# Optimization experiments

Measured on AMD Instinct MI355X. Metric: run time of the kernel, lower is better.

Reference implementation:

```python
import jax, jax.numpy as jnp
import numpy as np

N_HEADS = 8
OUT_DIM = 256   # node_dim + time_dim
KEY_DIM = 384   # node_dim + edge_dim + time_dim
HEAD_DIM = OUT_DIM // N_HEADS
LN_EPS = 1e-5


def setup_inputs() -> dict:
    key = jax.random.key(0)
    ks = jax.random.split(key, 12)
    B, N, D = 8192, 32, 128
    s = lambda fan_in: 1.0 / np.sqrt(fan_in)
    return {
        "node_feat": jax.random.normal(ks[0], (B, D), jnp.float32),
        "time_feat": jax.random.normal(ks[1], (B, D), jnp.float32),
        "edge_feat": jax.random.normal(ks[2], (B, N, D), jnp.float32),
        "nbr_node_feat": jax.random.normal(ks[3], (B, N, D), jnp.float32),
        "nbr_time_feat": jax.random.normal(ks[4], (B, N, D), jnp.float32),
        "nbr_mask": jax.random.randint(ks[5], (B, N), 0, 2, jnp.int64),
        # parameters, stored as [in, out] so y = x @ W
        "W_Q": jax.random.uniform(ks[6], (OUT_DIM, OUT_DIM), jnp.float32, -s(OUT_DIM), s(OUT_DIM)),
        "W_KV": jax.random.uniform(ks[7], (KEY_DIM, 2 * OUT_DIM), jnp.float32, -s(KEY_DIM), s(KEY_DIM)),
        "W_O": jax.random.uniform(ks[8], (OUT_DIM, OUT_DIM), jnp.float32, -s(OUT_DIM), s(OUT_DIM)),
        "b_O": jax.random.uniform(ks[9], (OUT_DIM,), jnp.float32, -s(OUT_DIM), s(OUT_DIM)),
        "ln_gamma": jnp.ones((OUT_DIM,), jnp.float32),
        "ln_beta": jnp.zeros((OUT_DIM,), jnp.float32),
    }


def reference(node_feat, time_feat, edge_feat, nbr_node_feat, nbr_time_feat,
              nbr_mask, W_Q, W_KV, W_O, b_O, ln_gamma, ln_beta):
    B = node_feat.shape[0]
    # query/residual: [B, out_dim] (query length is 1)
    R = jnp.concatenate([node_feat, time_feat], axis=1)
    Q = (R @ W_Q).reshape(B, N_HEADS, HEAD_DIM)                    # [B,H,d]
    Z = jnp.concatenate([nbr_node_feat, edge_feat, nbr_time_feat], axis=-1) @ W_KV  # [B,N,2*out]
    K = Z[:, :, :OUT_DIM].reshape(B, -1, N_HEADS, HEAD_DIM)        # [B,N,H,d]
    V = Z[:, :, OUT_DIM:].reshape(B, -1, N_HEADS, HEAD_DIM)
    A = jnp.einsum("bhd,bnhd->bhn", Q, K) * (HEAD_DIM ** -0.5)    # [B,H,N]
    masked = (nbr_mask == 0)[:, None, :]                           # [B,1,N]
    A = jnp.where(masked, jnp.float32(-1e10), A)
    A = jax.nn.softmax(A, axis=-1)                                 # dropout is identity (eval / p used at inference off)
    O = jnp.einsum("bhn,bnhd->bhd", A, V).reshape(B, OUT_DIM)
    out = O @ W_O + b_O
    x = out + R
    mu = jnp.mean(x, axis=-1, keepdims=True)
    var = jnp.mean(jnp.square(x - mu), axis=-1, keepdims=True)
    return (x - mu) * jax.lax.rsqrt(var + LN_EPS) * ln_gamma + ln_beta
```

## Files before the change

kernel.cpp:

```cpp
#include <hip/hip_runtime.h>

typedef __attribute__((ext_vector_type(8))) short bf16x8;
typedef __attribute__((ext_vector_type(4))) float f32x4;

#define MSTRIDE 264
#define XSTRIDE 392

__device__ __align__(16) unsigned short g_WQT[256 * 256];
__device__ __align__(16) unsigned short g_WKVT[512 * 384];
__device__ __align__(16) unsigned short g_WOT[256 * 256];

__device__ __forceinline__ float b2f(unsigned short u) {
    union { unsigned int i; float f; } v; v.i = ((unsigned int)u) << 16; return v.f;
}
__device__ __forceinline__ unsigned short f2b(float f) {
    union { float f; unsigned int i; } v; v.f = f;
    unsigned int x = v.i;
    return (unsigned short)((x + 0x7fffu + ((x >> 16) & 1u)) >> 16);
}

__global__ void transcvt_all(const float* __restrict__ wq, const float* __restrict__ wkv,
                             const float* __restrict__ wo,
                             unsigned short* __restrict__ dq, unsigned short* __restrict__ dkv,
                             unsigned short* __restrict__ dwo) {
    __shared__ float tile[32][33];
    const int b = blockIdx.x;
    const float* src; unsigned short* dst; int R, C, bx, by;
    if (b < 64)       { src = wq;  dst = dq;  R = 256; C = 256; bx = b & 7;  by = b >> 3; }
    else if (b < 256) { const int t = b - 64;  src = wkv; dst = dkv; R = 384; C = 512; bx = t & 15; by = t >> 4; }
    else              { const int t = b - 256; src = wo;  dst = dwo; R = 256; C = 256; bx = t & 7;  by = t >> 3; }
    const int c0 = bx * 32, r0 = by * 32;
    const int tx = threadIdx.x, ty = threadIdx.y;
#pragma unroll
    for (int i = 0; i < 32; i += 8)
        tile[ty + i][tx] = src[(size_t)(r0 + ty + i) * C + (c0 + tx)];
    __syncthreads();
#pragma unroll
    for (int i = 0; i < 32; i += 8)
        dst[(size_t)(c0 + ty + i) * R + (r0 + tx)] = f2b(tile[tx][ty + i]);
}

__device__ __forceinline__ void ld8f(const float* __restrict__ s, unsigned short* dst) {
    const float4 a = *(const float4*)s;
    const float4 b = *(const float4*)(s + 4);
    unsigned short t[8];
    t[0] = f2b(a.x); t[1] = f2b(a.y); t[2] = f2b(a.z); t[3] = f2b(a.w);
    t[4] = f2b(b.x); t[5] = f2b(b.y); t[6] = f2b(b.z); t[7] = f2b(b.w);
    *(uint4*)dst = *(const uint4*)t;
}

__global__ __launch_bounds__(256, 2) void ta_fused(
    const float* __restrict__ node,
    const float* __restrict__ timef,
    const float* __restrict__ edge,
    const float* __restrict__ nbrnode,
    const float* __restrict__ nbrtime,
    const int* __restrict__ nmask,
    const float* __restrict__ bO,
    const float* __restrict__ gam,
    const float* __restrict__ bet,
    float* __restrict__ out)
{
    __shared__ __align__(16) unsigned short Xs[64 * XSTRIDE];
    __shared__ __align__(16) unsigned short Rb[16 * MSTRIDE];
    __shared__ __align__(16) unsigned short Ob[16 * MSTRIDE];
    __shared__ float Qs[2][256];
    __shared__ float lnb[2][256];
    __shared__ int   mk[2][32];

    const int gb0  = blockIdx.x * 2;
    const int tid  = threadIdx.x;
    const int w    = tid >> 6;
    const int lane = tid & 63;
    const int l15  = lane & 15;
    const int quad = lane >> 4;

    int orv = 0;
#pragma unroll
    for (int i = 1; i < 64; i += 2) orv |= nmask[i];
    const bool m64 = (orv == 0);

    {
        unsigned int* pO = (unsigned int*)Ob;
        for (int i = tid; i < 16 * MSTRIDE / 2; i += 256) pO[i] = 0u;
        unsigned int* pR = (unsigned int*)Rb;
        for (int i = tid + MSTRIDE; i < 16 * MSTRIDE / 2; i += 256) pR[i] = 0u;
    }
    if (tid < 64) {
        const int b = tid >> 5, s = tid & 31;
        if (s < 16) ld8f(node  + (size_t)(gb0 + b) * 128 + s * 8,        &Rb[b * MSTRIDE + s * 8]);
        else        ld8f(timef + (size_t)(gb0 + b) * 128 + (s - 16) * 8, &Rb[b * MSTRIDE + s * 8]);
    } else if (tid < 128) {
        const int t = tid - 64, b = t >> 5, n = t & 31;
        const size_t j = (size_t)(gb0 + b) * 32 + n;
        mk[b][n] = m64 ? nmask[2 * j] : nmask[j];
    }
#pragma unroll
    for (int i = 0; i < 12; i++) {
        const int g  = i * 256 + tid;
        const int r  = g / 48, c8 = g % 48;
        const float* base; int koff;
        if (c8 < 16)      { base = nbrnode; koff = c8 * 8; }
        else if (c8 < 32) { base = edge;    koff = (c8 - 16) * 8; }
        else              { base = nbrtime; koff = (c8 - 32) * 8; }
        ld8f(base + (size_t)(gb0 * 32 + r) * 128 + koff, &Xs[r * XSTRIDE + c8 * 8]);
    }

    const unsigned short* wq  = g_WQT  + (size_t)(w * 64 + l15) * 256 + quad * 8;
    const unsigned short* wkv = g_WKVT + (size_t)(w * 64 + l15) * 384 + quad * 8;
    const unsigned short* wo  = g_WOT  + (size_t)(w * 64 + l15) * 256 + quad * 8;
    bf16x8 bq[2][4], bK[2][4], bV[2][4];
#pragma unroll
    for (int p = 0; p < 2; p++)
#pragma unroll
        for (int ct = 0; ct < 4; ct++)
            bq[p][ct] = *(const bf16x8*)(wq + (size_t)(ct * 16) * 256 + p * 32);
#pragma unroll
    for (int ct = 0; ct < 4; ct++) {
        bK[0][ct] = *(const bf16x8*)(wkv + (size_t)(ct * 16) * 384);
        bV[0][ct] = *(const bf16x8*)(wkv + (size_t)(256 + ct * 16) * 384);
    }

    __syncthreads();

    const f32x4 zero4 = {0.0f, 0.0f, 0.0f, 0.0f};

    f32x4 accq[4];
#pragma unroll
    for (int ct = 0; ct < 4; ct++) accq[ct] = zero4;
    {
        bf16x8 aq[2];
        aq[0] = *(const bf16x8*)(&Rb[l15 * MSTRIDE + 0 * 32 + quad * 8]);
        aq[1] = *(const bf16x8*)(&Rb[l15 * MSTRIDE + 1 * 32 + quad * 8]);
#pragma unroll
        for (int kc = 0; kc < 8; kc++) {
            const int s = kc & 1;
#pragma unroll
            for (int ct = 0; ct < 4; ct++)
                accq[ct] = __builtin_amdgcn_mfma_f32_16x16x32_bf16(aq[s], bq[s][ct], accq[ct], 0, 0, 0);
            if (kc + 2 < 8) {
                aq[s] = *(const bf16x8*)(&Rb[l15 * MSTRIDE + (kc + 2) * 32 + quad * 8]);
#pragma unroll
                for (int ct = 0; ct < 4; ct++)
                    bq[s][ct] = *(const bf16x8*)(wq + (size_t)(ct * 16) * 256 + (kc + 2) * 32);
            }
        }
    }
    if (quad == 0) {
#pragma unroll
        for (int ct = 0; ct < 4; ct++) {
            Qs[0][w * 64 + ct * 16 + l15] = accq[ct][0];
            Qs[1][w * 64 + ct * 16 + l15] = accq[ct][1];
        }
    }

    f32x4 accK[4][4], accV[4][4];
#pragma unroll
    for (int rt = 0; rt < 4; rt++)
#pragma unroll
        for (int ct = 0; ct < 4; ct++) { accK[rt][ct] = zero4; accV[rt][ct] = zero4; }
    {
        bf16x8 af[2][4];
#pragma unroll
        for (int rt = 0; rt < 4; rt++)
            af[0][rt] = *(const bf16x8*)(&Xs[(rt * 16 + l15) * XSTRIDE + quad * 8]);
#pragma unroll
        for (int ct = 0; ct < 4; ct++) {
            bK[1][ct] = *(const bf16x8*)(wkv + (size_t)(ct * 16) * 384 + 32);
            bV[1][ct] = *(const bf16x8*)(wkv + (size_t)(256 + ct * 16) * 384 + 32);
        }
#pragma unroll
        for (int kc = 0; kc < 12; kc++) {
            const int s = kc & 1;
            if (kc + 1 < 12) {
#pragma unroll
                for (int rt = 0; rt < 4; rt++)
                    af[s ^ 1][rt] = *(const bf16x8*)(&Xs[(rt * 16 + l15) * XSTRIDE + (kc + 1) * 32 + quad * 8]);
            }
            __builtin_amdgcn_s_setprio(1);
#pragma unroll
            for (int ct = 0; ct < 4; ct++)
#pragma unroll
                for (int rt = 0; rt < 4; rt++) {
                    accK[rt][ct] = __builtin_amdgcn_mfma_f32_16x16x32_bf16(af[s][rt], bK[s][ct], accK[rt][ct], 0, 0, 0);
                    accV[rt][ct] = __builtin_amdgcn_mfma_f32_16x16x32_bf16(af[s][rt], bV[s][ct], accV[rt][ct], 0, 0, 0);
                }
            __builtin_amdgcn_s_setprio(0);
            if (kc + 2 < 12) {
#pragma unroll
                for (int ct = 0; ct < 4; ct++) {
                    bK[s][ct] = *(const bf16x8*)(wkv + (size_t)(ct * 16) * 384 + (kc + 2) * 32);
                    bV[s][ct] = *(const bf16x8*)(wkv + (size_t)(256 + ct * 16) * 384 + (kc + 2) * 32);
                }
            }
        }
    }

    bf16x8 bo[2][4];
#pragma unroll
    for (int p = 0; p < 2; p++)
#pragma unroll
        for (int ct = 0; ct < 4; ct++)
            bo[p][ct] = *(const bf16x8*)(wo + (size_t)(ct * 16) * 256 + p * 32);

    float aw[2][2][2][4];
    const float scl = 0.17677669529663687f;
#pragma unroll
    for (int bb = 0; bb < 2; bb++) {
        float qv[4];
#pragma unroll
        for (int ct = 0; ct < 4; ct++) qv[ct] = Qs[bb][w * 64 + ct * 16 + l15];
#pragma unroll
        for (int hl = 0; hl < 2; hl++) {
            float sv[2][4];
#pragma unroll
            for (int rtl = 0; rtl < 2; rtl++) {
                const int rt = bb * 2 + rtl;
#pragma unroll
                for (int rg = 0; rg < 4; rg++)
                    sv[rtl][rg] = accK[rt][2 * hl][rg] * qv[2 * hl]
                                + accK[rt][2 * hl + 1][rg] * qv[2 * hl + 1];
            }
#pragma unroll
            for (int m = 1; m <= 8; m <<= 1)
#pragma unroll
                for (int rtl = 0; rtl < 2; rtl++)
#pragma unroll
                    for (int rg = 0; rg < 4; rg++)
                        sv[rtl][rg] += __shfl_xor(sv[rtl][rg], m, 64);
            float mx = -3.0e38f;
#pragma unroll
            for (int rtl = 0; rtl < 2; rtl++)
#pragma unroll
                for (int rg = 0; rg < 4; rg++) {
                    const int n = rtl * 16 + quad * 4 + rg;
                    sv[rtl][rg] = (mk[bb][n] != 0) ? sv[rtl][rg] * scl : -1.0e10f;
                    mx = fmaxf(mx, sv[rtl][rg]);
                }
            mx = fmaxf(mx, __shfl_xor(mx, 16, 64));
            mx = fmaxf(mx, __shfl_xor(mx, 32, 64));
            float sum = 0.0f;
#pragma unroll
            for (int rtl = 0; rtl < 2; rtl++)
#pragma unroll
                for (int rg = 0; rg < 4; rg++) {
                    const float e = __expf(sv[rtl][rg] - mx);
                    aw[bb][hl][rtl][rg] = e;
                    sum += e;
                }
            sum += __shfl_xor(sum, 16, 64);
            sum += __shfl_xor(sum, 32, 64);
            const float inv = 1.0f / sum;
#pragma unroll
            for (int rtl = 0; rtl < 2; rtl++)
#pragma unroll
                for (int rg = 0; rg < 4; rg++)
                    aw[bb][hl][rtl][rg] *= inv;
        }
    }

#pragma unroll
    for (int bb = 0; bb < 2; bb++)
#pragma unroll
        for (int hl = 0; hl < 2; hl++)
#pragma unroll
            for (int ctl = 0; ctl < 2; ctl++) {
                const int ct = hl * 2 + ctl;
                float o = 0.0f;
#pragma unroll
                for (int rtl = 0; rtl < 2; rtl++)
#pragma unroll
                    for (int rg = 0; rg < 4; rg++)
                        o += aw[bb][hl][rtl][rg] * accV[bb * 2 + rtl][ct][rg];
                o += __shfl_xor(o, 16, 64);
                o += __shfl_xor(o, 32, 64);
                if (quad == 0) {
                    const int col = (w * 2 + hl) * 32 + ctl * 16 + l15;
                    Ob[bb * MSTRIDE + col] = f2b(o);
                }
            }
    __syncthreads();

    f32x4 acco[4];
#pragma unroll
    for (int ct = 0; ct < 4; ct++) acco[ct] = zero4;
    {
        bf16x8 ao[2];
        ao[0] = *(const bf16x8*)(&Ob[l15 * MSTRIDE + 0 * 32 + quad * 8]);
        ao[1] = *(const bf16x8*)(&Ob[l15 * MSTRIDE + 1 * 32 + quad * 8]);
#pragma unroll
        for (int kc = 0; kc < 8; kc++) {
            const int s = kc & 1;
#pragma unroll
            for (int ct = 0; ct < 4; ct++)
                acco[ct] = __builtin_amdgcn_mfma_f32_16x16x32_bf16(ao[s], bo[s][ct], acco[ct], 0, 0, 0);
            if (kc + 2 < 8) {
                ao[s] = *(const bf16x8*)(&Ob[l15 * MSTRIDE + (kc + 2) * 32 + quad * 8]);
#pragma unroll
                for (int ct = 0; ct < 4; ct++)
                    bo[s][ct] = *(const bf16x8*)(wo + (size_t)(ct * 16) * 256 + (kc + 2) * 32);
            }
        }
    }
    if (quad == 0) {
#pragma unroll
        for (int ct = 0; ct < 4; ct++) {
#pragma unroll
            for (int r = 0; r < 2; r++) {
                const int col = w * 64 + ct * 16 + l15;
                lnb[r][col] = acco[ct][r] + bO[col] + b2f(Rb[r * MSTRIDE + col]);
            }
        }
    }
    __syncthreads();

    if (w < 2) {
        const int bb = w;
        float x[4]; float s = 0.0f;
#pragma unroll
        for (int i = 0; i < 4; i++) { x[i] = lnb[bb][lane + i * 64]; s += x[i]; }
#pragma unroll
        for (int m = 1; m <= 32; m <<= 1) s += __shfl_xor(s, m, 64);
        const float mu = s * (1.0f / 256.0f);
        float s2 = 0.0f;
#pragma unroll
        for (int i = 0; i < 4; i++) { const float d = x[i] - mu; s2 += d * d; }
#pragma unroll
        for (int m = 1; m <= 32; m <<= 1) s2 += __shfl_xor(s2, m, 64);
        const float rstd = rsqrtf(s2 * (1.0f / 256.0f) + 1e-5f);
#pragma unroll
        for (int i = 0; i < 4; i++) {
            const int col = lane + i * 64;
            out[(size_t)(gb0 + bb) * 256 + col] =
                (x[i] - mu) * rstd * gam[col] + bet[col];
        }
    }
}

extern "C" void kernel_launch(void* const* d_in, const int* in_sizes, int n_in,
                              void* d_out, int out_size, void* d_ws, size_t ws_size,
                              hipStream_t stream) {
    const float* node    = (const float*)d_in[0];
    const float* timef   = (const float*)d_in[1];
    const float* edge    = (const float*)d_in[2];
    const float* nbrnode = (const float*)d_in[3];
    const float* nbrtime = (const float*)d_in[4];
    const int*   nmask   = (const int*)d_in[5];
    const float* W_Q     = (const float*)d_in[6];
    const float* W_KV    = (const float*)d_in[7];
    const float* W_O     = (const float*)d_in[8];
    const float* bO      = (const float*)d_in[9];
    const float* gam     = (const float*)d_in[10];
    const float* bet     = (const float*)d_in[11];

    unsigned short *wqt, *wkvt, *wot;
    hipGetSymbolAddress((void**)&wqt,  HIP_SYMBOL(g_WQT));
    hipGetSymbolAddress((void**)&wkvt, HIP_SYMBOL(g_WKVT));
    hipGetSymbolAddress((void**)&wot,  HIP_SYMBOL(g_WOT));

    transcvt_all<<<320, dim3(32, 8), 0, stream>>>(W_Q, W_KV, W_O, wqt, wkvt, wot);

    ta_fused<<<4096, 256, 0, stream>>>(node, timef, edge, nbrnode, nbrtime, nmask,
                                       bO, gam, bet, (float*)d_out);
}
```

Baseline: 666.0 us.

## Split K and V projections and shrink LDS to fit three blocks per CU

The fused K/V GEMM is split into two separate passes, so only one set of 16 accumulator tiles is live at a time. V is now computed after the softmax. Query and output A-tiles are trimmed from 16 padded rows to 2 rows, Q is passed through shuffles instead of shared memory, and the LayerNorm buffer aliases the X tile. Together these cut register and LDS usage so launch bounds can ask for 3 blocks per CU. The cost is that the X tile is read from LDS twice and each k-step now has an s_barrier, which adds synchronisation.

```diff
diff --git a/kernel.cpp b/kernel.cpp
--- a/kernel.cpp
+++ b/kernel.cpp
@@ -49,7 +49,7 @@
     *(uint4*)dst = *(const uint4*)t;
 }
 
-__global__ __launch_bounds__(256, 2) void ta_fused(
+__global__ __launch_bounds__(256, 3) void ta_fused(
     const float* __restrict__ node,
     const float* __restrict__ timef,
     const float* __restrict__ edge,
@@ -62,11 +62,10 @@
     float* __restrict__ out)
 {
     __shared__ __align__(16) unsigned short Xs[64 * XSTRIDE];
-    __shared__ __align__(16) unsigned short Rb[16 * MSTRIDE];
-    __shared__ __align__(16) unsigned short Ob[16 * MSTRIDE];
-    __shared__ float Qs[2][256];
-    __shared__ float lnb[2][256];
-    __shared__ int   mk[2][32];
+    __shared__ __align__(16) unsigned short Rb[2 * MSTRIDE];
+    __shared__ __align__(16) unsigned short Ob[2 * MSTRIDE];
+    __shared__ int mk[2][32];
+    float* lnb = (float*)Xs;
 
     const int gb0  = blockIdx.x * 2;
     const int tid  = threadIdx.x;
@@ -74,18 +73,13 @@
     const int lane = tid & 63;
     const int l15  = lane & 15;
     const int quad = lane >> 4;
+    const int arow = (l15 & 1) * MSTRIDE;
 
     int orv = 0;
 #pragma unroll
     for (int i = 1; i < 64; i += 2) orv |= nmask[i];
     const bool m64 = (orv == 0);
 
-    {
-        unsigned int* pO = (unsigned int*)Ob;
-        for (int i = tid; i < 16 * MSTRIDE / 2; i += 256) pO[i] = 0u;
-        unsigned int* pR = (unsigned int*)Rb;
-        for (int i = tid + MSTRIDE; i < 16 * MSTRIDE / 2; i += 256) pR[i] = 0u;
-    }
     if (tid < 64) {
         const int b = tid >> 5, s = tid & 31;
         if (s < 16) ld8f(node  + (size_t)(gb0 + b) * 128 + s * 8,        &Rb[b * MSTRIDE + s * 8]);
@@ -105,103 +99,73 @@
         else              { base = nbrtime; koff = (c8 - 32) * 8; }
         ld8f(base + (size_t)(gb0 * 32 + r) * 128 + koff, &Xs[r * XSTRIDE + c8 * 8]);
     }
+    __syncthreads();
 
     const unsigned short* wq  = g_WQT  + (size_t)(w * 64 + l15) * 256 + quad * 8;
     const unsigned short* wkv = g_WKVT + (size_t)(w * 64 + l15) * 384 + quad * 8;
     const unsigned short* wo  = g_WOT  + (size_t)(w * 64 + l15) * 256 + quad * 8;
-    bf16x8 bq[2][4], bK[2][4], bV[2][4];
-#pragma unroll
-    for (int p = 0; p < 2; p++)
-#pragma unroll
-        for (int ct = 0; ct < 4; ct++)
-            bq[p][ct] = *(const bf16x8*)(wq + (size_t)(ct * 16) * 256 + p * 32);
-#pragma unroll
-    for (int ct = 0; ct < 4; ct++) {
-        bK[0][ct] = *(const bf16x8*)(wkv + (size_t)(ct * 16) * 384);
-        bV[0][ct] = *(const bf16x8*)(wkv + (size_t)(256 + ct * 16) * 384);
-    }
-
-    __syncthreads();
-
     const f32x4 zero4 = {0.0f, 0.0f, 0.0f, 0.0f};
 
     f32x4 accq[4];
 #pragma unroll
     for (int ct = 0; ct < 4; ct++) accq[ct] = zero4;
     {
-        bf16x8 aq[2];
-        aq[0] = *(const bf16x8*)(&Rb[l15 * MSTRIDE + 0 * 32 + quad * 8]);
-        aq[1] = *(const bf16x8*)(&Rb[l15 * MSTRIDE + 1 * 32 + quad * 8]);
+        bf16x8 bq[2][4];
+#pragma unroll
+        for (int p = 0; p < 2; p++)
+#pragma unroll
+            for (int ct = 0; ct < 4; ct++)
+                bq[p][ct] = *(const bf16x8*)(wq + (size_t)(ct * 16) * 256 + p * 32);
 #pragma unroll
         for (int kc = 0; kc < 8; kc++) {
             const int s = kc & 1;
-#pragma unroll
-            for (int ct = 0; ct < 4; ct++)
-                accq[ct] = __builtin_amdgcn_mfma_f32_16x16x32_bf16(aq[s], bq[s][ct], accq[ct], 0, 0, 0);
+            __builtin_amdgcn_s_barrier();
+            const bf16x8 aq = *(const bf16x8*)(&Rb[arow + kc * 32 + quad * 8]);
+#pragma unroll
+            for (int ct = 0; ct < 4; ct++)
+                accq[ct] = __builtin_amdgcn_mfma_f32_16x16x32_bf16(aq, bq[s][ct], accq[ct], 0, 0, 0);
             if (kc + 2 < 8) {
-                aq[s] = *(const bf16x8*)(&Rb[l15 * MSTRIDE + (kc + 2) * 32 + quad * 8]);
 #pragma unroll
                 for (int ct = 0; ct < 4; ct++)
                     bq[s][ct] = *(const bf16x8*)(wq + (size_t)(ct * 16) * 256 + (kc + 2) * 32);
             }
         }
     }
-    if (quad == 0) {
-#pragma unroll
-        for (int ct = 0; ct < 4; ct++) {
-            Qs[0][w * 64 + ct * 16 + l15] = accq[ct][0];
-            Qs[1][w * 64 + ct * 16 + l15] = accq[ct][1];
-        }
-    }
-
-    f32x4 accK[4][4], accV[4][4];
+
+    f32x4 accK[4][4];
 #pragma unroll
     for (int rt = 0; rt < 4; rt++)
 #pragma unroll
-        for (int ct = 0; ct < 4; ct++) { accK[rt][ct] = zero4; accV[rt][ct] = zero4; }
+        for (int ct = 0; ct < 4; ct++) accK[rt][ct] = zero4;
     {
-        bf16x8 af[2][4];
-#pragma unroll
-        for (int rt = 0; rt < 4; rt++)
-            af[0][rt] = *(const bf16x8*)(&Xs[(rt * 16 + l15) * XSTRIDE + quad * 8]);
-#pragma unroll
-        for (int ct = 0; ct < 4; ct++) {
-            bK[1][ct] = *(const bf16x8*)(wkv + (size_t)(ct * 16) * 384 + 32);
-            bV[1][ct] = *(const bf16x8*)(wkv + (size_t)(256 + ct * 16) * 384 + 32);
-        }
+        bf16x8 bK[2][4];
+#pragma unroll
+        for (int p = 0; p < 2; p++)
+#pragma unroll
+            for (int ct = 0; ct < 4; ct++)
+                bK[p][ct] = *(const bf16x8*)(wkv + (size_t)(ct * 16) * 384 + p * 32);
 #pragma unroll
         for (int kc = 0; kc < 12; kc++) {
             const int s = kc & 1;
-            if (kc + 1 < 12) {
+            __builtin_amdgcn_s_barrier();
+            bf16x8 af[4];
+#pragma unroll
+            for (int rt = 0; rt < 4; rt++)
+                af[rt] = *(const bf16x8*)(&Xs[(rt * 16 + l15) * XSTRIDE + kc * 32 + quad * 8]);
+            __builtin_amdgcn_s_setprio(1);
+#pragma unroll
+            for (int ct = 0; ct < 4; ct++)
 #pragma unroll
                 for (int rt = 0; rt < 4; rt++)
-                    af[s ^ 1][rt] = *(const bf16x8*)(&Xs[(rt * 16 + l15) * XSTRIDE + (kc + 1) * 32 + quad * 8]);
-            }
-            __builtin_amdgcn_s_setprio(1);
-#pragma unroll
-            for (int ct = 0; ct < 4; ct++)
-#pragma unroll
-                for (int rt = 0; rt < 4; rt++) {
-                    accK[rt][ct] = __builtin_amdgcn_mfma_f32_16x16x32_bf16(af[s][rt], bK[s][ct], accK[rt][ct], 0, 0, 0);
-                    accV[rt][ct] = __builtin_amdgcn_mfma_f32_16x16x32_bf16(af[s][rt], bV[s][ct], accV[rt][ct], 0, 0, 0);
-                }
+                    accK[rt][ct] = __builtin_amdgcn_mfma_f32_16x16x32_bf16(af[rt], bK[s][ct], accK[rt][ct], 0, 0, 0);
             __builtin_amdgcn_s_setprio(0);
             if (kc + 2 < 12) {
 #pragma unroll
-                for (int ct = 0; ct < 4; ct++) {
+                for (int ct = 0; ct < 4; ct++)
                     bK[s][ct] = *(const bf16x8*)(wkv + (size_t)(ct * 16) * 384 + (kc + 2) * 32);
-                    bV[s][ct] = *(const bf16x8*)(wkv + (size_t)(256 + ct * 16) * 384 + (kc + 2) * 32);
-                }
-            }
-        }
-    }
-
-    bf16x8 bo[2][4];
-#pragma unroll
-    for (int p = 0; p < 2; p++)
-#pragma unroll
-        for (int ct = 0; ct < 4; ct++)
-            bo[p][ct] = *(const bf16x8*)(wo + (size_t)(ct * 16) * 256 + p * 32);
+            }
+        }
+    }
 
     float aw[2][2][2][4];
     const float scl = 0.17677669529663687f;
@@ -209,7 +173,7 @@
     for (int bb = 0; bb < 2; bb++) {
         float qv[4];
 #pragma unroll
-        for (int ct = 0; ct < 4; ct++) qv[ct] = Qs[bb][w * 64 + ct * 16 + l15];
+        for (int ct = 0; ct < 4; ct++) qv[ct] = __shfl(accq[ct][bb], l15, 64);
 #pragma unroll
         for (int hl = 0; hl < 2; hl++) {
             float sv[2][4];
@@ -259,6 +223,41 @@
         }
     }
 
+    f32x4 accV[4][4];
+#pragma unroll
+    for (int rt = 0; rt < 4; rt++)
+#pragma unroll
+        for (int ct = 0; ct < 4; ct++) accV[rt][ct] = zero4;
+    {
+        bf16x8 bV[2][4];
+#pragma unroll
+        for (int p = 0; p < 2; p++)
+#pragma unroll
+            for (int ct = 0; ct < 4; ct++)
+                bV[p][ct] = *(const bf16x8*)(wkv + (size_t)(256 + ct * 16) * 384 + p * 32);
+#pragma unroll
+        for (int kc = 0; kc < 12; kc++) {
+            const int s = kc & 1;
+            __builtin_amdgcn_s_barrier();
+            bf16x8 af[4];
+#pragma unroll
+            for (int rt = 0; rt < 4; rt++)
+                af[rt] = *(const bf16x8*)(&Xs[(rt * 16 + l15) * XSTRIDE + kc * 32 + quad * 8]);
+            __builtin_amdgcn_s_setprio(1);
+#pragma unroll
+            for (int ct = 0; ct < 4; ct++)
+#pragma unroll
+                for (int rt = 0; rt < 4; rt++)
+                    accV[rt][ct] = __builtin_amdgcn_mfma_f32_16x16x32_bf16(af[rt], bV[s][ct], accV[rt][ct], 0, 0, 0);
+            __builtin_amdgcn_s_setprio(0);
+            if (kc + 2 < 12) {
+#pragma unroll
+                for (int ct = 0; ct < 4; ct++)
+                    bV[s][ct] = *(const bf16x8*)(wkv + (size_t)(256 + ct * 16) * 384 + (kc + 2) * 32);
+            }
+        }
+    }
+
 #pragma unroll
     for (int bb = 0; bb < 2; bb++)
 #pragma unroll
@@ -285,17 +284,21 @@
 #pragma unroll
     for (int ct = 0; ct < 4; ct++) acco[ct] = zero4;
     {
-        bf16x8 ao[2];
-        ao[0] = *(const bf16x8*)(&Ob[l15 * MSTRIDE + 0 * 32 + quad * 8]);
-        ao[1] = *(const bf16x8*)(&Ob[l15 * MSTRIDE + 1 * 32 + quad * 8]);
+        bf16x8 bo[2][4];
+#pragma unroll
+        for (int p = 0; p < 2; p++)
+#pragma unroll
+            for (int ct = 0; ct < 4; ct++)
+                bo[p][ct] = *(const bf16x8*)(wo + (size_t)(ct * 16) * 256 + p * 32);
 #pragma unroll
         for (int kc = 0; kc < 8; kc++) {
             const int s = kc & 1;
-#pragma unroll
-            for (int ct = 0; ct < 4; ct++)
-                acco[ct] = __builtin_amdgcn_mfma_f32_16x16x32_bf16(ao[s], bo[s][ct], acco[ct], 0, 0, 0);
+            __builtin_amdgcn_s_barrier();
+            const bf16x8 ao = *(const bf16x8*)(&Ob[arow + kc * 32 + quad * 8]);
+#pragma unroll
+            for (int ct = 0; ct < 4; ct++)
+                acco[ct] = __builtin_amdgcn_mfma_f32_16x16x32_bf16(ao, bo[s][ct], acco[ct], 0, 0, 0);
             if (kc + 2 < 8) {
-                ao[s] = *(const bf16x8*)(&Ob[l15 * MSTRIDE + (kc + 2) * 32 + quad * 8]);
 #pragma unroll
                 for (int ct = 0; ct < 4; ct++)
                     bo[s][ct] = *(const bf16x8*)(wo + (size_t)(ct * 16) * 256 + (kc + 2) * 32);
@@ -308,7 +311,7 @@
 #pragma unroll
             for (int r = 0; r < 2; r++) {
                 const int col = w * 64 + ct * 16 + l15;
-                lnb[r][col] = acco[ct][r] + bO[col] + b2f(Rb[r * MSTRIDE + col]);
+                lnb[r * 256 + col] = acco[ct][r] + bO[col] + b2f(Rb[r * MSTRIDE + col]);
             }
         }
     }
@@ -318,7 +321,7 @@
         const int bb = w;
         float x[4]; float s = 0.0f;
 #pragma unroll
-        for (int i = 0; i < 4; i++) { x[i] = lnb[bb][lane + i * 64]; s += x[i]; }
+        for (int i = 0; i < 4; i++) { x[i] = lnb[bb * 256 + lane + i * 64]; s += x[i]; }
 #pragma unroll
         for (int m = 1; m <= 32; m <<= 1) s += __shfl_xor(s, m, 64);
         const float mu = s * (1.0f / 256.0f);
```

New measurement: 665.2 us. Within noise of the previous version (-0.1%).
